# Kernel optimization log

Hardware: AMD Instinct MI355X
Metric: run time of the kernel (lower is better)

Reference implementation:

```python
import jax, jax.numpy as jnp
import numpy as np

HIDDEN = 2048
GAMMA = 0.96875
SCALE_BASE = 512  # XPOS default from torchscale / Jamie-Stirling/RetNet


def _xpos(x, downscale=False):
    # x: [B, L, d]. Faithful port of XPOS with offset=0.
    B, L, d = x.shape
    half = d // 2
    # per-dim scale vector: (arange(0,d,2) + 0.4d) / (1.4d)
    scale_vec = (jnp.arange(0, d, 2, dtype=jnp.float32) + 0.4 * d) / (1.4 * d)  # [half]
    power = jnp.arange(L, dtype=jnp.float32) / SCALE_BASE                        # [L]
    scale = scale_vec[None, :] ** power[:, None]                                 # [L, half]
    # fixed_pos_embedding over `half` frequency dims
    inv_freq = 1.0 / (10000.0 ** (jnp.arange(half, dtype=jnp.float32) / half))   # [half]
    sinusoid = jnp.arange(L, dtype=jnp.float32)[:, None] * inv_freq[None, :]     # [L, half]
    sin, cos = jnp.sin(sinusoid), jnp.cos(sinusoid)
    if downscale:
        scale = 1.0 / scale
    # duplicate_interleave: [L, half] -> [L, d] with each column repeated twice
    sin_s = jnp.repeat(sin * scale, 2, axis=-1)  # [L, d]
    cos_s = jnp.repeat(cos * scale, 2, axis=-1)  # [L, d]
    # rotate_every_two
    x1 = x[..., 0::2]
    x2 = x[..., 1::2]
    rot = jnp.stack((-x2, x1), axis=-1).reshape(x.shape)
    return x * cos_s[None] + rot * sin_s[None]


def _decay_matrix(L):
    n = jnp.arange(L)[:, None]
    m = jnp.arange(L)[None, :]
    mask = n >= m
    # clamp exponent to avoid overflow where masked (torch sets NaN->0)
    D = jnp.where(mask, GAMMA ** jnp.maximum(n - m, 0).astype(jnp.float32), 0.0)
    return D  # [L, L]


def setup_inputs() -> dict:
    key = jax.random.key(0)
    kx, kq, kk, kv = jax.random.split(key, 4)
    B, S, H = 4, 2048, HIDDEN
    X = jax.random.normal(kx, (B, S, H), dtype=jnp.float32)
    W_Q = jax.random.normal(kq, (H, H), dtype=jnp.float32) / H
    W_K = jax.random.normal(kk, (H, H), dtype=jnp.float32) / H
    W_V = jax.random.normal(kv, (H, H), dtype=jnp.float32) / H
    return {"X": X, "W_Q": W_Q, "W_K": W_K, "W_V": W_V}


def reference(X, W_Q, W_K, W_V):
    B, S, H = X.shape
    Q = _xpos(X @ W_Q)                   # [B, S, H]
    K = _xpos(X @ W_K, downscale=True)   # [B, S, H]
    V = X @ W_V                          # [B, S, H]
    D = _decay_matrix(S)                 # [S, S]
    att = jnp.einsum("bnh,bmh->bnm", Q, K) * D[None]  # [B, S, S]
    return att @ V                       # [B, S, H]
```

## Files before the change

kernel.cpp:

```cpp
#include <hip/hip_runtime.h>
#include <math.h>


typedef __attribute__((ext_vector_type(8))) short short8;
typedef __attribute__((ext_vector_type(4))) float f32x4;
typedef __attribute__((ext_vector_type(4))) unsigned short us4;

#define BM 256
#define BN 256
#define BK 64

static __device__ __forceinline__ unsigned short f2bf(float f) {
    unsigned int u = __float_as_uint(f);
    u += 0x7FFFu + ((u >> 16) & 1u);
    return (unsigned short)(u >> 16);
}

static __device__ __forceinline__ void gload16(const unsigned short* g, unsigned short* l) {
    __builtin_amdgcn_global_load_lds(
        (const __attribute__((address_space(1))) unsigned int*)g,
        (__attribute__((address_space(3))) unsigned int*)l, 16, 0, 0);
}

template <int STAGE>
__global__ __launch_bounds__(512, 2)
void gemm_bt(const unsigned short* __restrict__ A,
             const unsigned short* __restrict__ Bt,
             void* __restrict__ Cv,
             unsigned short* __restrict__ Cq,
             unsigned short* __restrict__ Ck,
             unsigned short* __restrict__ Cvt,
             int lda, int ldb, int Kd,
             long long sA, long long sB, long long sC)
{
    constexpr int S = 2048, H = 2048;
    const int rowBase = blockIdx.y * BM;
    const int colBase = blockIdx.x * BN;

    if (STAGE == 3 && blockIdx.x > blockIdx.y) return;

    A  += (long long)blockIdx.z * sA;
    Bt += (long long)blockIdx.z * sB;

    __shared__ unsigned short As[2 * BM * BK];
    __shared__ unsigned short Bs[2 * BN * BK];

    const int tid  = threadIdx.x;
    const int wave = tid >> 6;
    const int lane = tid & 63;
    const int wm = (wave >> 2) * 128;
    const int wn = (wave & 3) * 64;

    f32x4 acc[8][4];
#pragma unroll
    for (int i = 0; i < 8; ++i)
#pragma unroll
        for (int j = 0; j < 4; ++j) acc[i][j] = (f32x4){0.f, 0.f, 0.f, 0.f};

    int kmax = Kd;
    if (STAGE == 4) kmax = rowBase + BM;

    const int srow = wave * 32 + (lane >> 3);
    const int schunk = ((lane & 7) ^ ((lane >> 3) & 7)) * 8;
    const unsigned short* ga = A  + (size_t)(rowBase + srow) * lda + schunk;
    const unsigned short* gb = Bt + (size_t)(colBase + srow) * ldb + schunk;
    unsigned short* lA0 = As + wave * 2048;
    unsigned short* lB0 = Bs + wave * 2048;

    const int fr  = lane & 15;
    const int qd  = lane >> 4;
    const int fsw = fr & 7;
    const int nt  = kmax >> 6;

#pragma unroll
    for (int g = 0; g < 4; ++g) {
        gload16(ga + (size_t)g * 8 * lda, lA0 + g * 512);
        gload16(gb + (size_t)g * 8 * ldb, lB0 + g * 512);
    }

    for (int t = 0; t < nt; ++t) {
        const int b = t & 1;
        if (t + 1 < nt) {
            const unsigned short* gA = ga + (t + 1) * BK;
            const unsigned short* gB = gb + (t + 1) * BK;
            unsigned short* lA = lA0 + (b ^ 1) * 16384;
            unsigned short* lB = lB0 + (b ^ 1) * 16384;
#pragma unroll
            for (int g = 0; g < 4; ++g) {
                gload16(gA + (size_t)g * 8 * lda, lA + g * 512);
                gload16(gB + (size_t)g * 8 * ldb, lB + g * 512);
            }
            __builtin_amdgcn_sched_barrier(0);
            asm volatile("s_waitcnt vmcnt(8)" ::: "memory");
        } else {
            __builtin_amdgcn_sched_barrier(0);
            asm volatile("s_waitcnt vmcnt(0)" ::: "memory");
        }
        __builtin_amdgcn_sched_barrier(0);
        __builtin_amdgcn_s_barrier();
        asm volatile("" ::: "memory");

        const unsigned short* Ab = As + b * 16384;
        const unsigned short* Bb = Bs + b * 16384;
#pragma unroll
        for (int kk = 0; kk < 2; ++kk) {
            short8 bfr[4], afr[8];
#pragma unroll
            for (int j = 0; j < 4; ++j) {
                int row = wn + j * 16 + fr;
                bfr[j] = *(const short8*)&Bb[row * 64 + (((kk * 4 + qd) ^ fsw) * 8)];
            }
#pragma unroll
            for (int i = 0; i < 8; ++i) {
                int row = wm + i * 16 + fr;
                afr[i] = *(const short8*)&Ab[row * 64 + (((kk * 4 + qd) ^ fsw) * 8)];
            }
#pragma unroll
            for (int i = 0; i < 8; ++i)
#pragma unroll
                for (int j = 0; j < 4; ++j)
                    acc[i][j] = __builtin_amdgcn_mfma_f32_16x16x32_bf16(afr[i], bfr[j], acc[i][j], 0, 0, 0);
        }
        asm volatile("" ::: "memory");
        __builtin_amdgcn_s_barrier();
    }

    if (STAGE == 1) {
        const int mode = colBase >> 11;
        if (mode < 2) {
            unsigned short* Co = (mode == 0) ? Cq : Ck;
            const float psgn = (mode == 1) ? -1.953125e-3f : 1.953125e-3f;
#pragma unroll
            for (int j = 0; j < 4; ++j) {
                int gc = (colBase & 2047) + wn + j * 16 + fr;
                float c0 = (float)(gc & ~1);
                float l2sv = log2f((c0 + 819.2f) * (1.0f / 2867.2f)) * psgn;
                float invf = exp2f(c0 * -0.0064881407f);
                float s1, c1;
                sincosf(invf, &s1, &c1);
#pragma unroll
                for (int i = 0; i < 8; ++i) {
                    int gr0 = rowBase + wm + i * 16 + qd * 4;
                    float fn = (float)(gr0 & (S - 1));
                    float sN, cN;
                    sincosf(fn * invf, &sN, &cN);
#pragma unroll
                    for (int r = 0; r < 4; ++r) {
                        float scale = exp2f(fn * l2sv);
                        float cs = cN * scale, ss = sN * scale;
                        float v = acc[i][j][r];
                        float o = __shfl_xor(v, 1);
                        float res = (gc & 1) ? fmaf(v, cs, o * ss) : fmaf(v, cs, -o * ss);
                        Co[(size_t)(gr0 + r) * H + gc] = f2bf(res);
                        float sn2 = sN * c1 + cN * s1;
                        cN = cN * c1 - sN * s1;
                        sN = sn2;
                        fn += 1.0f;
                    }
                }
            }
        } else {
#pragma unroll
            for (int j = 0; j < 4; ++j) {
                int gh = (colBase & 2047) + wn + j * 16 + fr;
#pragma unroll
                for (int i = 0; i < 8; ++i) {
                    int gm0 = rowBase + wm + i * 16 + qd * 4;
                    us4 p;
#pragma unroll
                    for (int r = 0; r < 4; ++r) p[r] = f2bf(acc[i][j][r]);
                    *(us4*)&Cvt[(size_t)gh * 8192 + gm0] = p;
                }
            }
        }
    } else if (STAGE == 3) {
        unsigned short* att = (unsigned short*)Cv + (long long)blockIdx.z * sC;
#pragma unroll
        for (int j = 0; j < 4; ++j) {
            int m = colBase + wn + j * 16 + fr;
#pragma unroll
            for (int i = 0; i < 8; ++i) {
                int n0 = rowBase + wm + i * 16 + qd * 4;
#pragma unroll
                for (int r = 0; r < 4; ++r) {
                    int d = n0 + r - m;
                    float v = (d >= 0) ? acc[i][j][r] * exp2f((float)d * -0.045803598f) : 0.0f;
                    att[(size_t)(n0 + r) * S + m] = f2bf(v);
                }
            }
        }
    } else {
        float* Co = (float*)Cv + (long long)blockIdx.z * sC;
#pragma unroll
        for (int j = 0; j < 4; ++j) {
            int gh = colBase + wn + j * 16 + fr;
#pragma unroll
            for (int i = 0; i < 8; ++i) {
                int gn0 = rowBase + wm + i * 16 + qd * 4;
#pragma unroll
                for (int r = 0; r < 4; ++r)
                    Co[(size_t)(gn0 + r) * H + gh] = acc[i][j][r];
            }
        }
    }
}

__global__ __launch_bounds__(256)
void cvt_f32_bf16(const float* __restrict__ x, unsigned short* __restrict__ y) {
    int i = blockIdx.x * 256 + threadIdx.x;
    float4 v = ((const float4*)x)[i];
    us4 o = {f2bf(v.x), f2bf(v.y), f2bf(v.z), f2bf(v.w)};
    ((us4*)y)[i] = o;
}

__global__ __launch_bounds__(256)
void cvt_transpose3(const float* __restrict__ W0, const float* __restrict__ W1,
                    const float* __restrict__ W2, unsigned short* __restrict__ Wt) {
    __shared__ float t[64][65];
    const float* W = (blockIdx.z == 0) ? W0 : (blockIdx.z == 1) ? W1 : W2;
    unsigned short* Wo = Wt + (size_t)blockIdx.z * 4194304;
    int bx = blockIdx.x * 64, by = blockIdx.y * 64;
    int tx = threadIdx.x & 63, ty = threadIdx.x >> 6;
#pragma unroll
    for (int r = 0; r < 64; r += 4)
        t[ty + r][tx] = W[(size_t)(by + ty + r) * 2048 + bx + tx];
    __syncthreads();
#pragma unroll
    for (int r = 0; r < 64; r += 4)
        Wo[(size_t)(bx + ty + r) * 2048 + by + tx] = f2bf(t[tx][ty + r]);
}

extern "C" void kernel_launch(void* const* d_in, const int* in_sizes, int n_in,
                              void* d_out, int out_size, void* d_ws, size_t ws_size,
                              hipStream_t stream) {
    const int S = 2048, H = 2048;
    const long long MH = 16777216;
    const long long HH = 4194304;
    const long long SH = (long long)S * H;
    const long long SS = (long long)S * S;

    const float* X  = (const float*)d_in[0];
    const float* WQ = (const float*)d_in[1];
    const float* WK = (const float*)d_in[2];
    const float* WV = (const float*)d_in[3];
    float* out = (float*)d_out;

    unsigned short* Xb    = (unsigned short*)d_ws;
    unsigned short* WtAll = Xb + MH;
    unsigned short* Qb    = WtAll + 3 * HH;
    unsigned short* Kb    = Qb + MH;
    unsigned short* Vt    = Kb + MH;
    unsigned short* att   = Vt + MH;

    cvt_f32_bf16<<<16384, 256, 0, stream>>>(X, Xb);
    cvt_transpose3<<<dim3(32, 32, 3), 256, 0, stream>>>(WQ, WK, WV, WtAll);

    gemm_bt<1><<<dim3(24, 32), 512, 0, stream>>>(Xb, WtAll, nullptr, Qb, Kb, Vt,
                                                 H, H, H, 0, 0, 0);
    gemm_bt<3><<<dim3(8, 8, 4), 512, 0, stream>>>(Qb, Kb, att, nullptr, nullptr, nullptr,
                                                  H, H, H, SH, SH, SS);
    gemm_bt<4><<<dim3(8, 8, 4), 512, 0, stream>>>(att, Vt, out, nullptr, nullptr, nullptr,
                                                  S, 8192, S, SS, 2048, SH);
}
```

Measured before the change: 516.3 us.

## Restructure GEMM main loop into fine-grained half-K stages with interleaved prefetch

Splits each 64-wide K tile into two 32-wide LDS sub-buffers and reworks the main loop into four MFMA phases. Each phase is separated by barriers and issues one quarter of the global-to-LDS prefetch, looking up to two tiles ahead. It also raises wave priority with s_setprio around the MFMA bursts and changes the XOR swizzle to a 4-chunk pattern. The goal is to hide global load latency and LDS read stalls behind matrix ops. In exchange it adds many more barriers per tile and depends on delicate vmcnt accounting.

```diff
diff --git a/kernel.cpp b/kernel.cpp
--- a/kernel.cpp
+++ b/kernel.cpp
@@ -42,8 +42,8 @@
     A  += (long long)blockIdx.z * sA;
     Bt += (long long)blockIdx.z * sB;
 
-    __shared__ unsigned short As[2 * BM * BK];
-    __shared__ unsigned short Bs[2 * BN * BK];
+    __shared__ unsigned short As[32768];
+    __shared__ unsigned short Bs[32768];
 
     const int tid  = threadIdx.x;
     const int wave = tid >> 6;
@@ -59,71 +59,113 @@
 
     int kmax = Kd;
     if (STAGE == 4) kmax = rowBase + BM;
-
-    const int srow = wave * 32 + (lane >> 3);
-    const int schunk = ((lane & 7) ^ ((lane >> 3) & 7)) * 8;
-    const unsigned short* ga = A  + (size_t)(rowBase + srow) * lda + schunk;
-    const unsigned short* gb = Bt + (size_t)(colBase + srow) * ldb + schunk;
-    unsigned short* lA0 = As + wave * 2048;
-    unsigned short* lB0 = Bs + wave * 2048;
-
-    const int fr  = lane & 15;
-    const int qd  = lane >> 4;
-    const int fsw = fr & 7;
-    const int nt  = kmax >> 6;
-
-#pragma unroll
-    for (int g = 0; g < 4; ++g) {
-        gload16(ga + (size_t)g * 8 * lda, lA0 + g * 512);
-        gload16(gb + (size_t)g * 8 * ldb, lB0 + g * 512);
-    }
+    const int nt = kmax >> 6;
+
+    const int lr  = lane >> 2;
+    const int sc8 = ((lane & 3) ^ ((lane >> 3) & 3)) * 8;
+    const unsigned short* gaS = A  + (size_t)(rowBase + wave * 32 + lr) * lda + sc8;
+    const unsigned short* gbS = Bt + (size_t)(colBase + wave * 32 + lr) * ldb + sc8;
+    unsigned short* lAw = As + wave * 1024;
+    unsigned short* lBw = Bs + wave * 1024;
+
+    const int fr = lane & 15;
+    const int qd = lane >> 4;
+    const int cq = (qd ^ ((fr >> 1) & 3)) * 8;
+
+#define STG_A(t, kk, buf) do { \
+    const unsigned short* _g = gaS + (t) * 64 + (kk) * 32; \
+    unsigned short* _l = lAw + ((buf) * 2 + (kk)) * 8192; \
+    gload16(_g, _l); gload16(_g + (size_t)16 * lda, _l + 512); } while (0)
+#define STG_B(t, kk, buf) do { \
+    const unsigned short* _g = gbS + (t) * 64 + (kk) * 32; \
+    unsigned short* _l = lBw + ((buf) * 2 + (kk)) * 8192; \
+    gload16(_g, _l); gload16(_g + (size_t)16 * ldb, _l + 512); } while (0)
+
+    STG_A(0, 0, 0); STG_B(0, 0, 0); STG_A(0, 1, 0); STG_B(0, 1, 0);
+    STG_A(1, 0, 1); STG_B(1, 0, 1); STG_A(1, 1, 1);
+    __builtin_amdgcn_sched_barrier(0);
+    asm volatile("s_waitcnt vmcnt(6)" ::: "memory");
+    __builtin_amdgcn_sched_barrier(0);
+    __builtin_amdgcn_s_barrier();
 
     for (int t = 0; t < nt; ++t) {
         const int b = t & 1;
-        if (t + 1 < nt) {
-            const unsigned short* gA = ga + (t + 1) * BK;
-            const unsigned short* gB = gb + (t + 1) * BK;
-            unsigned short* lA = lA0 + (b ^ 1) * 16384;
-            unsigned short* lB = lB0 + (b ^ 1) * 16384;
-#pragma unroll
-            for (int g = 0; g < 4; ++g) {
-                gload16(gA + (size_t)g * 8 * lda, lA + g * 512);
-                gload16(gB + (size_t)g * 8 * ldb, lB + g * 512);
-            }
-            __builtin_amdgcn_sched_barrier(0);
-            asm volatile("s_waitcnt vmcnt(8)" ::: "memory");
-        } else {
-            __builtin_amdgcn_sched_barrier(0);
-            asm volatile("s_waitcnt vmcnt(0)" ::: "memory");
-        }
+        const unsigned short* Ab0 = As + (b * 2 + 0) * 8192;
+        const unsigned short* Bb0 = Bs + (b * 2 + 0) * 8192;
+        const unsigned short* Ab1 = As + (b * 2 + 1) * 8192;
+        const unsigned short* Bb1 = Bs + (b * 2 + 1) * 8192;
+        const bool pf1 = (t + 1 < nt);
+        const bool pf2 = (t + 2 < nt);
+        short8 af[8], bf0, bf1;
+
+#pragma unroll
+        for (int i = 0; i < 8; ++i)
+            af[i] = *(const short8*)&Ab0[(wm + i * 16 + fr) * 32 + cq];
+        bf0 = *(const short8*)&Bb0[(wn + 0 * 16 + fr) * 32 + cq];
+        bf1 = *(const short8*)&Bb0[(wn + 1 * 16 + fr) * 32 + cq];
+        if (pf1) STG_B(t + 1, 1, b ^ 1);
+        __builtin_amdgcn_s_barrier();
+        asm volatile("s_waitcnt lgkmcnt(0)" ::: "memory");
+        __builtin_amdgcn_s_setprio(1);
+#pragma unroll
+        for (int i = 0; i < 8; ++i) {
+            acc[i][0] = __builtin_amdgcn_mfma_f32_16x16x32_bf16(af[i], bf0, acc[i][0], 0, 0, 0);
+            acc[i][1] = __builtin_amdgcn_mfma_f32_16x16x32_bf16(af[i], bf1, acc[i][1], 0, 0, 0);
+        }
+        __builtin_amdgcn_s_setprio(0);
+        __builtin_amdgcn_s_barrier();
+
+        bf0 = *(const short8*)&Bb0[(wn + 2 * 16 + fr) * 32 + cq];
+        bf1 = *(const short8*)&Bb0[(wn + 3 * 16 + fr) * 32 + cq];
+        if (pf2) STG_A(t + 2, 0, b);
+        __builtin_amdgcn_s_barrier();
+        asm volatile("s_waitcnt lgkmcnt(0)" ::: "memory");
+        __builtin_amdgcn_s_setprio(1);
+#pragma unroll
+        for (int i = 0; i < 8; ++i) {
+            acc[i][2] = __builtin_amdgcn_mfma_f32_16x16x32_bf16(af[i], bf0, acc[i][2], 0, 0, 0);
+            acc[i][3] = __builtin_amdgcn_mfma_f32_16x16x32_bf16(af[i], bf1, acc[i][3], 0, 0, 0);
+        }
+        __builtin_amdgcn_s_setprio(0);
+        __builtin_amdgcn_s_barrier();
+
+#pragma unroll
+        for (int i = 0; i < 8; ++i)
+            af[i] = *(const short8*)&Ab1[(wm + i * 16 + fr) * 32 + cq];
+        bf0 = *(const short8*)&Bb1[(wn + 0 * 16 + fr) * 32 + cq];
+        bf1 = *(const short8*)&Bb1[(wn + 1 * 16 + fr) * 32 + cq];
+        if (pf2) STG_B(t + 2, 0, b);
+        __builtin_amdgcn_s_barrier();
+        asm volatile("s_waitcnt lgkmcnt(0)" ::: "memory");
+        __builtin_amdgcn_s_setprio(1);
+#pragma unroll
+        for (int i = 0; i < 8; ++i) {
+            acc[i][0] = __builtin_amdgcn_mfma_f32_16x16x32_bf16(af[i], bf0, acc[i][0], 0, 0, 0);
+            acc[i][1] = __builtin_amdgcn_mfma_f32_16x16x32_bf16(af[i], bf1, acc[i][1], 0, 0, 0);
+        }
+        __builtin_amdgcn_s_setprio(0);
+        __builtin_amdgcn_s_barrier();
+
+        bf0 = *(const short8*)&Bb1[(wn + 2 * 16 + fr) * 32 + cq];
+        bf1 = *(const short8*)&Bb1[(wn + 3 * 16 + fr) * 32 + cq];
+        if (pf2) STG_A(t + 2, 1, b);
         __builtin_amdgcn_sched_barrier(0);
-        __builtin_amdgcn_s_barrier();
-        asm volatile("" ::: "memory");
-
-        const unsigned short* Ab = As + b * 16384;
-        const unsigned short* Bb = Bs + b * 16384;
-#pragma unroll
-        for (int kk = 0; kk < 2; ++kk) {
-            short8 bfr[4], afr[8];
-#pragma unroll
-            for (int j = 0; j < 4; ++j) {
-                int row = wn + j * 16 + fr;
-                bfr[j] = *(const short8*)&Bb[row * 64 + (((kk * 4 + qd) ^ fsw) * 8)];
-            }
-#pragma unroll
-            for (int i = 0; i < 8; ++i) {
-                int row = wm + i * 16 + fr;
-                afr[i] = *(const short8*)&Ab[row * 64 + (((kk * 4 + qd) ^ fsw) * 8)];
-            }
-#pragma unroll
-            for (int i = 0; i < 8; ++i)
-#pragma unroll
-                for (int j = 0; j < 4; ++j)
-                    acc[i][j] = __builtin_amdgcn_mfma_f32_16x16x32_bf16(afr[i], bfr[j], acc[i][j], 0, 0, 0);
-        }
-        asm volatile("" ::: "memory");
+        if (pf2) { asm volatile("s_waitcnt vmcnt(6)" ::: "memory"); }
+        else     { asm volatile("s_waitcnt vmcnt(0)" ::: "memory"); }
+        __builtin_amdgcn_sched_barrier(0);
+        __builtin_amdgcn_s_barrier();
+        asm volatile("s_waitcnt lgkmcnt(0)" ::: "memory");
+        __builtin_amdgcn_s_setprio(1);
+#pragma unroll
+        for (int i = 0; i < 8; ++i) {
+            acc[i][2] = __builtin_amdgcn_mfma_f32_16x16x32_bf16(af[i], bf0, acc[i][2], 0, 0, 0);
+            acc[i][3] = __builtin_amdgcn_mfma_f32_16x16x32_bf16(af[i], bf1, acc[i][3], 0, 0, 0);
+        }
+        __builtin_amdgcn_s_setprio(0);
         __builtin_amdgcn_s_barrier();
     }
+#undef STG_A
+#undef STG_B
 
     if (STAGE == 1) {
         const int mode = colBase >> 11;
```

Measured after the change: 527.7 us. 2.2% more time.
